# Kernel tuning notes

Hardware: AMD Instinct MI355X
Metric: run time of the kernel (lower is better)

Reference implementation:

```python
import jax, jax.numpy as jnp
import numpy as np

C = 64          # number of concepts (output_size)
MC = 100        # num_monte_carlo
TRI = C * (C + 1) // 2
ROWS, COLS = np.tril_indices(C)          # static lower-triangular indices
DIAG_MASK = ROWS == COLS                 # positions in c_sigma that are diagonal
DIAG = np.arange(C)


def setup_inputs() -> dict:
    key = jax.random.key(0)
    k_x, k_eps, k_wmu, k_wsig = jax.random.split(key, 4)
    B, F = 4096, 512
    return {
        "x": jax.random.normal(k_x, (B, F), jnp.float32),
        "eps": jax.random.normal(k_eps, (B, C, MC), jnp.float32),  # MVN standard-normal draws
        "w_mu": jax.random.normal(k_wmu, (C, F), jnp.float32) / np.float32(np.sqrt(F)),
        "b_mu": jnp.zeros((C,), jnp.float32),
        # sigma.weight.data *= 0.01 in the original module
        "w_sigma": jax.random.normal(k_wsig, (TRI, F), jnp.float32) * np.float32(0.01 / np.sqrt(F)),
        "b_sigma": jnp.zeros((TRI,), jnp.float32),
    }


def reference(x, eps, w_mu, b_mu, w_sigma, b_sigma):
    # mu head: Linear(F -> C)
    c_mu = x @ w_mu.T + b_mu                          # [B, C]
    # sigma head: Linear(F -> C*(C+1)/2)
    c_sigma = x @ w_sigma.T + b_sigma                 # [B, TRI]

    B = x.shape[0]
    # build lower-triangular scale matrix (predict_sigma)
    L = jnp.zeros((B, C, C), x.dtype)
    L = L.at[:, ROWS, COLS].set(c_sigma)
    diag_vals = jax.nn.softplus(c_sigma[:, DIAG_MASK]) + 1e-6
    L = L.at[:, DIAG, DIAG].set(diag_vals)            # [B, C, C]

    # MVN rsample([MC]) with scale_tril L: sample = mu + L @ eps
    logits = c_mu[:, :, None] + jnp.einsum('bij,bjm->bim', L, eps)  # [B, C, MC]
    return jax.nn.sigmoid(logits)
```

## Files before the change

kernel.cpp:

```cpp
#include <hip/hip_runtime.h>
#include <hip/hip_bf16.h>


typedef short bf16x8 __attribute__((ext_vector_type(8)));
typedef float f32x4 __attribute__((ext_vector_type(4)));

__device__ __forceinline__ unsigned short f2bf(float f) {
    union { float f; unsigned u; } u; u.f = f;
    unsigned r = u.u + 0x7FFFu + ((u.u >> 16) & 1u);
    return (unsigned short)(r >> 16);
}

__device__ __forceinline__ int swz(int r) { return (r ^ (r >> 3)) & 7; }

__device__ __forceinline__ void tri_ij(int t, int& i, int& j) {
    i = (int)((sqrtf((float)(8 * t + 1)) - 1.0f) * 0.5f);
    if ((i + 1) * (i + 2) / 2 <= t) ++i;
    if (i * (i + 1) / 2 > t) --i;
    j = t - ((i * (i + 1)) >> 1);
}

__device__ __forceinline__ void gload16(const void* g, void* l) {
    __builtin_amdgcn_global_load_lds(
        (const __attribute__((address_space(1))) void*)g,
        (__attribute__((address_space(3))) void*)l, 16, 0, 0);
}

__global__ __launch_bounds__(256) void cvt_kernel(
    const float* __restrict__ x, const float* __restrict__ wmu,
    const float* __restrict__ wsig,
    unsigned short* __restrict__ Xb, unsigned short* __restrict__ Wb) {
    const int NX = (4096 * 512) / 4;
    const int NW = (2144 * 512) / 4;
    const int NMU = (64 * 512) / 4;
    int tot = NX + NW;
    for (int i = blockIdx.x * blockDim.x + threadIdx.x; i < tot;
         i += gridDim.x * blockDim.x) {
        float4 v; unsigned short* dst;
        if (i < NX) {
            v = ((const float4*)x)[i];
            dst = Xb + (size_t)i * 4;
        } else {
            int j = i - NX;
            if (j < NMU) v = ((const float4*)wmu)[j];
            else         v = ((const float4*)wsig)[j - NMU];
            dst = Wb + (size_t)j * 4;
        }
        ushort4 o;
        o.x = f2bf(v.x); o.y = f2bf(v.y); o.z = f2bf(v.z); o.w = f2bf(v.w);
        *(ushort4*)dst = o;
    }
}

__global__ __launch_bounds__(256) void gemm_kernel(
    const unsigned short* __restrict__ Xb, const unsigned short* __restrict__ Wb,
    const float* __restrict__ bmu, const float* __restrict__ bsig,
    float* __restrict__ Mu, unsigned short* __restrict__ Sg) {
    __shared__ __align__(16) unsigned short smem[16384];

    int flat = blockIdx.y * 17 + blockIdx.x;
    int virt = (flat & 7) * 68 + (flat >> 3);
    int vbx = virt % 17, vby = virt / 17;
    int r0 = vby * 128, c0 = vbx * 128;

    int tid = threadIdx.x;
    int w = tid >> 6, lane = tid & 63;
    int wr = w >> 1, wc = w & 1;
    int lr = lane & 15, kg = lane >> 4;

    int sr = tid >> 3;
    int sc = tid & 7;
    int scx = sc ^ (sr & 7);
    const unsigned short* Ag = Xb + (size_t)(r0 + sr) * 512 + scx * 8;
    const unsigned short* Bg = Wb + (size_t)(c0 + sr) * 512 + scx * 8;
    unsigned short* As = smem + tid * 8;
    unsigned short* Bs = smem + 8192 + tid * 8;

    f32x4 acc[4][4];
    #pragma unroll
    for (int i = 0; i < 4; ++i)
        #pragma unroll
        for (int j = 0; j < 4; ++j) acc[i][j] = (f32x4){0.f, 0.f, 0.f, 0.f};

    for (int kt = 0; kt < 8; ++kt) {
        int k0 = kt * 64;
        #pragma unroll
        for (int i = 0; i < 4; ++i) {
            gload16(Ag + (size_t)i * 32 * 512 + k0, As + i * 2048);
            gload16(Bg + (size_t)i * 32 * 512 + k0, Bs + i * 2048);
        }
        __syncthreads();
        #pragma unroll
        for (int h = 0; h < 2; ++h) {
            bf16x8 a[4], bv[4];
            #pragma unroll
            for (int i = 0; i < 4; ++i) {
                int row = wr * 64 + i * 16 + lr;
                int ch = ((h << 2) | kg) ^ (row & 7);
                a[i] = *(const bf16x8*)(smem + row * 64 + ch * 8);
            }
            #pragma unroll
            for (int j = 0; j < 4; ++j) {
                int row = wc * 64 + j * 16 + lr;
                int ch = ((h << 2) | kg) ^ (row & 7);
                bv[j] = *(const bf16x8*)(smem + 8192 + row * 64 + ch * 8);
            }
            #pragma unroll
            for (int i = 0; i < 4; ++i)
                #pragma unroll
                for (int j = 0; j < 4; ++j)
                    acc[i][j] = __builtin_amdgcn_mfma_f32_16x16x32_bf16(
                        a[i], bv[j], acc[i][j], 0, 0, 0);
        }
        __syncthreads();
    }

    int rbase = r0 + wr * 64 + (kg << 2);
    #pragma unroll
    for (int j = 0; j < 4; ++j) {
        int col = c0 + wc * 64 + j * 16 + lr;
        if (col < 64) {
            float bias = bmu[col];
            #pragma unroll
            for (int i = 0; i < 4; ++i)
                #pragma unroll
                for (int r = 0; r < 4; ++r)
                    Mu[(size_t)(rbase + i * 16 + r) * 64 + col] = acc[i][j][r] + bias;
        } else if (col < 2144) {
            int t = col - 64;
            float bias = bsig[t];
            int ti, tj; tri_ij(t, ti, tj);
            bool dg = (tj == ti);
            #pragma unroll
            for (int i = 0; i < 4; ++i) {
                #pragma unroll
                for (int r = 0; r < 4; ++r) {
                    float v = acc[i][j][r] + bias;
                    if (dg) v = (v > 15.f ? v : __logf(1.f + __expf(v))) + 1e-6f;
                    Sg[(size_t)(rbase + i * 16 + r) * 2080 + t] = f2bf(v);
                }
            }
        }
    }
}

__global__ __launch_bounds__(512, 6) void sample_kernel(
    const float* __restrict__ Mu, const unsigned short* __restrict__ Sg,
    const float* __restrict__ eps, float* __restrict__ out) {
    __shared__ __align__(16) unsigned short raw[2][2080];
    __shared__ __align__(16) unsigned short Lh[2][64][64];
    __shared__ __align__(16) float Ost[6400];

    int blk = blockIdx.x;
    int nb = (blk < 256) ? 6 : 5;

    int tid = threadIdx.x;
    int w = tid >> 6, lane = tid & 63;
    int lr = lane & 15, kg = lane >> 4;
    int m = (w << 4) + lr;
    int ml = (m < 100) ? m : 96;
    int m0 = (w << 4) + (kg << 2);
    bool cw = (w < 7);
    bool st = cw && (m0 < 100);

    if (tid < 260)
        gload16(Sg + (size_t)blk * 2080 + tid * 8, &raw[0][tid * 8]);

    float ef[16], mun[4], muc[4];
    bf16x8 a0, a1;

    __syncthreads();

    for (int k = 0; k <= nb; ++k) {
        int b = blk + k * 768;
        int cur = k & 1;

        if (k >= 1 && cw) {
            #pragma unroll
            for (int s = 0; s < 4; ++s) {
                __hip_bfloat162 h0 = __float22bfloat162_rn(
                    make_float2(ef[2 * s], ef[2 * s + 1]));
                __hip_bfloat162 h1 = __float22bfloat162_rn(
                    make_float2(ef[8 + 2 * s], ef[8 + 2 * s + 1]));
                ((unsigned*)&a0)[s] = *(unsigned*)&h0;
                ((unsigned*)&a1)[s] = *(unsigned*)&h1;
            }
            #pragma unroll
            for (int g = 0; g < 4; ++g) muc[g] = mun[g];
        }

        if (k < nb && cw) {
            const float* er = eps + (size_t)b * 6400;
            #pragma unroll
            for (int s = 0; s < 8; ++s) {
                ef[s]     = er[(kg * 8 + s) * 100 + ml];
                ef[s + 8] = er[(32 + kg * 8 + s) * 100 + ml];
            }
            #pragma unroll
            for (int g = 0; g < 4; ++g)
                mun[g] = Mu[((size_t)b << 6) + g * 16 + lr];
        }

        if (k + 1 < nb && tid < 260)
            gload16(Sg + (size_t)(b + 768) * 2080 + tid * 8, &raw[cur ^ 1][tid * 8]);

        if (k < nb) {
            #pragma unroll
            for (int kk = 0; kk < 4; ++kk) {
                int idx = tid + (kk << 9);
                int i = idx >> 5;
                int j0 = (idx & 31) << 1;
                unsigned u = 0u;
                if (j0 <= i) {
                    int t = ((i * (i + 1)) >> 1) + j0;
                    u = raw[cur][t];
                    if (j0 + 1 <= i) u |= ((unsigned)raw[cur][t + 1]) << 16;
                }
                *(unsigned*)&Lh[cur][i][(((j0 >> 3) ^ swz(i)) << 3) | (j0 & 7)] = u;
            }
        }

        if (k >= 1 && cw) {
            #pragma unroll
            for (int g = 0; g < 4; ++g) {
                int i = g * 16 + lr;
                int si = swz(i);
                bf16x8 L0 = *(const bf16x8*)&Lh[cur ^ 1][i][(kg ^ si) << 3];
                bf16x8 L1 = *(const bf16x8*)&Lh[cur ^ 1][i][((kg + 4) ^ si) << 3];
                f32x4 acc = {0.f, 0.f, 0.f, 0.f};
                acc = __builtin_amdgcn_mfma_f32_16x16x32_bf16(a0, L0, acc, 0, 0, 0);
                acc = __builtin_amdgcn_mfma_f32_16x16x32_bf16(a1, L1, acc, 0, 0, 0);
                if (st) {
                    float4 o;
                    #pragma unroll
                    for (int r = 0; r < 4; ++r) {
                        float z = muc[g] + acc[r];
                        ((float*)&o)[r] = __fdividef(1.f, 1.f + __expf(-z));
                    }
                    *(float4*)&Ost[i * 100 + m0] = o;
                }
            }
        }

        __syncthreads();

        if (k >= 1) {
            size_t ob = (size_t)(b - 768) * 6400;
            #pragma unroll
            for (int kk = 0; kk < 4; ++kk) {
                int f = tid + (kk << 9);
                if (f < 1600)
                    *(float4*)(out + ob + f * 4) = ((const float4*)Ost)[f];
            }
        }

        __syncthreads();
    }
}

extern "C" void kernel_launch(void* const* d_in, const int* in_sizes, int n_in,
                              void* d_out, int out_size, void* d_ws, size_t ws_size,
                              hipStream_t stream) {
    const float* x    = (const float*)d_in[0];
    const float* eps  = (const float*)d_in[1];
    const float* wmu  = (const float*)d_in[2];
    const float* bmu  = (const float*)d_in[3];
    const float* wsig = (const float*)d_in[4];
    const float* bsig = (const float*)d_in[5];
    float* out = (float*)d_out;

    char* ws = (char*)d_ws;
    unsigned short* Xb = (unsigned short*)ws;
    unsigned short* Wb = (unsigned short*)(ws + 4194304);
    float*          Mu = (float*)(ws + 4194304 + 2195456);
    unsigned short* Sg = (unsigned short*)(ws + 4194304 + 2195456 + 1048576);

    cvt_kernel<<<2048, 256, 0, stream>>>(x, wmu, wsig, Xb, Wb);
    gemm_kernel<<<dim3(17, 32), 256, 0, stream>>>(Xb, Wb, bmu, bsig, Mu, Sg);
    sample_kernel<<<768, 512, 0, stream>>>(Mu, Sg, eps, out);
}
```

Baseline: 94.86 us.

## Scatter sigma directly into dense zeroed L in global memory, one sample block per batch

The GEMM epilogue now writes each sigma entry straight into a dense 64x64 bf16 L matrix per batch row, and the convert kernel zero-fills that buffer first. The sample kernel then loads L fragments directly from global memory and runs one block per batch element. This removes the persistent double-buffered loop and the shared-memory triangle unpacking. In exchange the L buffer is about twice the size of the packed triangle, adding a 32MB zero-fill plus extra global traffic, and the sample kernel loses its cross-batch prefetch overlap.

```diff
diff --git a/kernel.cpp b/kernel.cpp
--- a/kernel.cpp
+++ b/kernel.cpp
@@ -10,8 +10,6 @@
     unsigned r = u.u + 0x7FFFu + ((u.u >> 16) & 1u);
     return (unsigned short)(r >> 16);
 }
-
-__device__ __forceinline__ int swz(int r) { return (r ^ (r >> 3)) & 7; }
 
 __device__ __forceinline__ void tri_ij(int t, int& i, int& j) {
     i = (int)((sqrtf((float)(8 * t + 1)) - 1.0f) * 0.5f);
@@ -29,33 +27,39 @@
 __global__ __launch_bounds__(256) void cvt_kernel(
     const float* __restrict__ x, const float* __restrict__ wmu,
     const float* __restrict__ wsig,
-    unsigned short* __restrict__ Xb, unsigned short* __restrict__ Wb) {
+    unsigned short* __restrict__ Xb, unsigned short* __restrict__ Wb,
+    uint4* __restrict__ Ldz) {
     const int NX = (4096 * 512) / 4;
     const int NW = (2144 * 512) / 4;
     const int NMU = (64 * 512) / 4;
-    int tot = NX + NW;
+    const int NZ = (4096 * 64 * 64 * 2) / 16;
+    int tot = NX + NW + NZ;
     for (int i = blockIdx.x * blockDim.x + threadIdx.x; i < tot;
          i += gridDim.x * blockDim.x) {
-        float4 v; unsigned short* dst;
-        if (i < NX) {
-            v = ((const float4*)x)[i];
-            dst = Xb + (size_t)i * 4;
+        if (i < NX + NW) {
+            float4 v; unsigned short* dst;
+            if (i < NX) {
+                v = ((const float4*)x)[i];
+                dst = Xb + (size_t)i * 4;
+            } else {
+                int j = i - NX;
+                if (j < NMU) v = ((const float4*)wmu)[j];
+                else         v = ((const float4*)wsig)[j - NMU];
+                dst = Wb + (size_t)j * 4;
+            }
+            ushort4 o;
+            o.x = f2bf(v.x); o.y = f2bf(v.y); o.z = f2bf(v.z); o.w = f2bf(v.w);
+            *(ushort4*)dst = o;
         } else {
-            int j = i - NX;
-            if (j < NMU) v = ((const float4*)wmu)[j];
-            else         v = ((const float4*)wsig)[j - NMU];
-            dst = Wb + (size_t)j * 4;
-        }
-        ushort4 o;
-        o.x = f2bf(v.x); o.y = f2bf(v.y); o.z = f2bf(v.z); o.w = f2bf(v.w);
-        *(ushort4*)dst = o;
+            Ldz[i - NX - NW] = make_uint4(0u, 0u, 0u, 0u);
+        }
     }
 }
 
 __global__ __launch_bounds__(256) void gemm_kernel(
     const unsigned short* __restrict__ Xb, const unsigned short* __restrict__ Wb,
     const float* __restrict__ bmu, const float* __restrict__ bsig,
-    float* __restrict__ Mu, unsigned short* __restrict__ Sg) {
+    float* __restrict__ Mu, unsigned short* __restrict__ Ld) {
     __shared__ __align__(16) unsigned short smem[16384];
 
     int flat = blockIdx.y * 17 + blockIdx.x;
@@ -131,29 +135,26 @@
             float bias = bsig[t];
             int ti, tj; tri_ij(t, ti, tj);
             bool dg = (tj == ti);
+            int ofs = ti * 64 + tj;
             #pragma unroll
             for (int i = 0; i < 4; ++i) {
                 #pragma unroll
                 for (int r = 0; r < 4; ++r) {
                     float v = acc[i][j][r] + bias;
                     if (dg) v = (v > 15.f ? v : __logf(1.f + __expf(v))) + 1e-6f;
-                    Sg[(size_t)(rbase + i * 16 + r) * 2080 + t] = f2bf(v);
+                    Ld[((size_t)(rbase + i * 16 + r) << 12) + ofs] = f2bf(v);
                 }
             }
         }
     }
 }
 
-__global__ __launch_bounds__(512, 6) void sample_kernel(
-    const float* __restrict__ Mu, const unsigned short* __restrict__ Sg,
+__global__ __launch_bounds__(512, 4) void sample_kernel(
+    const float* __restrict__ Mu, const unsigned short* __restrict__ Ld,
     const float* __restrict__ eps, float* __restrict__ out) {
-    __shared__ __align__(16) unsigned short raw[2][2080];
-    __shared__ __align__(16) unsigned short Lh[2][64][64];
     __shared__ __align__(16) float Ost[6400];
 
-    int blk = blockIdx.x;
-    int nb = (blk < 256) ? 6 : 5;
-
+    int b = blockIdx.x;
     int tid = threadIdx.x;
     int w = tid >> 6, lane = tid & 63;
     int lr = lane & 15, kg = lane >> 4;
@@ -163,98 +164,57 @@
     bool cw = (w < 7);
     bool st = cw && (m0 < 100);
 
-    if (tid < 260)
-        gload16(Sg + (size_t)blk * 2080 + tid * 8, &raw[0][tid * 8]);
-
-    float ef[16], mun[4], muc[4];
-    bf16x8 a0, a1;
+    if (cw) {
+        const float* er = eps + (size_t)b * 6400;
+        float ef[16];
+        #pragma unroll
+        for (int s = 0; s < 8; ++s) {
+            ef[s]     = er[(kg * 8 + s) * 100 + ml];
+            ef[s + 8] = er[(32 + kg * 8 + s) * 100 + ml];
+        }
+        float muv[4];
+        #pragma unroll
+        for (int g = 0; g < 4; ++g)
+            muv[g] = Mu[((size_t)b << 6) + g * 16 + lr];
+        bf16x8 a0, a1;
+        #pragma unroll
+        for (int s = 0; s < 4; ++s) {
+            __hip_bfloat162 h0 = __float22bfloat162_rn(
+                make_float2(ef[2 * s], ef[2 * s + 1]));
+            __hip_bfloat162 h1 = __float22bfloat162_rn(
+                make_float2(ef[8 + 2 * s], ef[8 + 2 * s + 1]));
+            ((unsigned*)&a0)[s] = *(unsigned*)&h0;
+            ((unsigned*)&a1)[s] = *(unsigned*)&h1;
+        }
+        const unsigned short* lb = Ld + ((size_t)b << 12);
+        #pragma unroll
+        for (int g = 0; g < 4; ++g) {
+            int i = g * 16 + lr;
+            bf16x8 L0 = *(const bf16x8*)(lb + i * 64 + kg * 8);
+            bf16x8 L1 = *(const bf16x8*)(lb + i * 64 + (kg + 4) * 8);
+            f32x4 acc = {0.f, 0.f, 0.f, 0.f};
+            acc = __builtin_amdgcn_mfma_f32_16x16x32_bf16(a0, L0, acc, 0, 0, 0);
+            acc = __builtin_amdgcn_mfma_f32_16x16x32_bf16(a1, L1, acc, 0, 0, 0);
+            if (st) {
+                float4 o;
+                #pragma unroll
+                for (int r = 0; r < 4; ++r) {
+                    float z = muv[g] + acc[r];
+                    ((float*)&o)[r] = __fdividef(1.f, 1.f + __expf(-z));
+                }
+                *(float4*)&Ost[i * 100 + m0] = o;
+            }
+        }
+    }
 
     __syncthreads();
 
-    for (int k = 0; k <= nb; ++k) {
-        int b = blk + k * 768;
-        int cur = k & 1;
-
-        if (k >= 1 && cw) {
-            #pragma unroll
-            for (int s = 0; s < 4; ++s) {
-                __hip_bfloat162 h0 = __float22bfloat162_rn(
-                    make_float2(ef[2 * s], ef[2 * s + 1]));
-                __hip_bfloat162 h1 = __float22bfloat162_rn(
-                    make_float2(ef[8 + 2 * s], ef[8 + 2 * s + 1]));
-                ((unsigned*)&a0)[s] = *(unsigned*)&h0;
-                ((unsigned*)&a1)[s] = *(unsigned*)&h1;
-            }
-            #pragma unroll
-            for (int g = 0; g < 4; ++g) muc[g] = mun[g];
-        }
-
-        if (k < nb && cw) {
-            const float* er = eps + (size_t)b * 6400;
-            #pragma unroll
-            for (int s = 0; s < 8; ++s) {
-                ef[s]     = er[(kg * 8 + s) * 100 + ml];
-                ef[s + 8] = er[(32 + kg * 8 + s) * 100 + ml];
-            }
-            #pragma unroll
-            for (int g = 0; g < 4; ++g)
-                mun[g] = Mu[((size_t)b << 6) + g * 16 + lr];
-        }
-
-        if (k + 1 < nb && tid < 260)
-            gload16(Sg + (size_t)(b + 768) * 2080 + tid * 8, &raw[cur ^ 1][tid * 8]);
-
-        if (k < nb) {
-            #pragma unroll
-            for (int kk = 0; kk < 4; ++kk) {
-                int idx = tid + (kk << 9);
-                int i = idx >> 5;
-                int j0 = (idx & 31) << 1;
-                unsigned u = 0u;
-                if (j0 <= i) {
-                    int t = ((i * (i + 1)) >> 1) + j0;
-                    u = raw[cur][t];
-                    if (j0 + 1 <= i) u |= ((unsigned)raw[cur][t + 1]) << 16;
-                }
-                *(unsigned*)&Lh[cur][i][(((j0 >> 3) ^ swz(i)) << 3) | (j0 & 7)] = u;
-            }
-        }
-
-        if (k >= 1 && cw) {
-            #pragma unroll
-            for (int g = 0; g < 4; ++g) {
-                int i = g * 16 + lr;
-                int si = swz(i);
-                bf16x8 L0 = *(const bf16x8*)&Lh[cur ^ 1][i][(kg ^ si) << 3];
-                bf16x8 L1 = *(const bf16x8*)&Lh[cur ^ 1][i][((kg + 4) ^ si) << 3];
-                f32x4 acc = {0.f, 0.f, 0.f, 0.f};
-                acc = __builtin_amdgcn_mfma_f32_16x16x32_bf16(a0, L0, acc, 0, 0, 0);
-                acc = __builtin_amdgcn_mfma_f32_16x16x32_bf16(a1, L1, acc, 0, 0, 0);
-                if (st) {
-                    float4 o;
-                    #pragma unroll
-                    for (int r = 0; r < 4; ++r) {
-                        float z = muc[g] + acc[r];
-                        ((float*)&o)[r] = __fdividef(1.f, 1.f + __expf(-z));
-                    }
-                    *(float4*)&Ost[i * 100 + m0] = o;
-                }
-            }
-        }
-
-        __syncthreads();
-
-        if (k >= 1) {
-            size_t ob = (size_t)(b - 768) * 6400;
-            #pragma unroll
-            for (int kk = 0; kk < 4; ++kk) {
-                int f = tid + (kk << 9);
-                if (f < 1600)
-                    *(float4*)(out + ob + f * 4) = ((const float4*)Ost)[f];
-            }
-        }
-
-        __syncthreads();
+    size_t ob = (size_t)b * 6400;
+    #pragma unroll
+    for (int kk = 0; kk < 4; ++kk) {
+        int f = tid + (kk << 9);
+        if (f < 1600)
+            *(float4*)(out + ob + f * 4) = ((const float4*)Ost)[f];
     }
 }
 
@@ -273,9 +233,9 @@
     unsigned short* Xb = (unsigned short*)ws;
     unsigned short* Wb = (unsigned short*)(ws + 4194304);
     float*          Mu = (float*)(ws + 4194304 + 2195456);
-    unsigned short* Sg = (unsigned short*)(ws + 4194304 + 2195456 + 1048576);
-
-    cvt_kernel<<<2048, 256, 0, stream>>>(x, wmu, wsig, Xb, Wb);
-    gemm_kernel<<<dim3(17, 32), 256, 0, stream>>>(Xb, Wb, bmu, bsig, Mu, Sg);
-    sample_kernel<<<768, 512, 0, stream>>>(Mu, Sg, eps, out);
-}
+    unsigned short* Ld = (unsigned short*)(ws + 7438336);
+
+    cvt_kernel<<<2048, 256, 0, stream>>>(x, wmu, wsig, Xb, Wb, (uint4*)Ld);
+    gemm_kernel<<<dim3(17, 32), 256, 0, stream>>>(Xb, Wb, bmu, bsig, Mu, Ld);
+    sample_kernel<<<4096, 512, 0, stream>>>(Mu, Ld, eps, out);
+}
```

After: 94.58 us. No clear change (-0.3%).
